# Kernel tuning notes

Hardware: AMD Instinct MI355X
Metric: run time of the kernel (lower is better)

The kernel has to match this reference:

```python
import jax, jax.numpy as jnp
import numpy as np
import math

DIM = 4096
N_HEADS = 32
N_KV_HEADS = 8
HEAD_DIM = DIM // N_HEADS          # 128
N_REP = N_HEADS // N_KV_HEADS      # 4
BATCH = 2
SEQ = 2048
ROPE_THETA = 10000.0


def rope_cos_sin(seq_len, head_dim, theta=ROPE_THETA):
    # matches precompute_freqs_cis: freqs over even indices, outer with positions
    inv_freq = 1.0 / (theta ** (jnp.arange(0, head_dim, 2, dtype=jnp.float32) / head_dim))
    t = jnp.arange(seq_len, dtype=jnp.float32)
    ang = jnp.outer(t, inv_freq)          # [S, head_dim//2]
    return jnp.cos(ang), jnp.sin(ang)


def apply_rope(x, cos, sin):
    # x: [B, S, H, D]; consecutive pairs (x0, x1) form complex numbers (view_as_complex)
    x0 = x[..., 0::2]
    x1 = x[..., 1::2]
    c = cos[None, :, None, :]
    s = sin[None, :, None, :]
    r0 = x0 * c - x1 * s
    r1 = x0 * s + x1 * c
    return jnp.stack([r0, r1], axis=-1).reshape(x.shape)


def setup_inputs() -> dict:
    key = jax.random.key(0)
    ks = jax.random.split(key, 5)
    scale = 1.0 / math.sqrt(DIM)
    return {
        "x": jax.random.normal(ks[0], (BATCH, SEQ, DIM), dtype=jnp.float32),
        "wq": jax.random.normal(ks[1], (DIM, N_HEADS * HEAD_DIM), dtype=jnp.float32) * scale,
        "wk": jax.random.normal(ks[2], (DIM, N_KV_HEADS * HEAD_DIM), dtype=jnp.float32) * scale,
        "wv": jax.random.normal(ks[3], (DIM, N_KV_HEADS * HEAD_DIM), dtype=jnp.float32) * scale,
        "wo": jax.random.normal(ks[4], (N_HEADS * HEAD_DIM, DIM), dtype=jnp.float32) * scale,
        "start_pos": 0,
    }


def reference(x, wq, wk, wv, wo, start_pos):
    B, S, _ = x.shape
    # projections
    q = (x @ wq).reshape(B, S, N_HEADS, HEAD_DIM)
    k = (x @ wk).reshape(B, S, N_KV_HEADS, HEAD_DIM)
    v = (x @ wv).reshape(B, S, N_KV_HEADS, HEAD_DIM)
    # RoPE on q, k (training path: full-sequence freqs)
    cos, sin = rope_cos_sin(S, HEAD_DIM)
    q = apply_rope(q, cos, sin)
    k = apply_rope(k, cos, sin)
    # GQA: repeat_kv expands kv heads by n_rep
    k = jnp.repeat(k, N_REP, axis=2)  # [B, S, H, D]
    v = jnp.repeat(v, N_REP, axis=2)
    # [B, H, S, D]
    q = q.transpose(0, 2, 1, 3)
    k = k.transpose(0, 2, 1, 3)
    v = v.transpose(0, 2, 1, 3)
    scores = jnp.einsum("bhqd,bhkd->bhqk", q, k) / math.sqrt(HEAD_DIM)
    # causal mask: -inf above diagonal
    mask = jnp.triu(jnp.full((S, S), float("-inf"), dtype=scores.dtype), k=1)
    scores = scores + mask[None, None]
    attn = jax.nn.softmax(scores.astype(jnp.float32), axis=-1).astype(q.dtype)
    out = jnp.einsum("bhqk,bhkd->bhqd", attn, v)
    out = out.transpose(0, 2, 1, 3).reshape(B, S, N_HEADS * HEAD_DIM)
    return out @ wo
```

## Files before the change

### kernel.cpp

```cpp
#include <hip/hip_runtime.h>

#define DIM 4096
#define HD 128
#define NH 32
#define NKV 8
#define SEQ 2048
#define BATCH 2
#define MTOT (BATCH*SEQ)
#define GK DIM

typedef __bf16 bf16;
typedef __bf16 bf16x4 __attribute__((ext_vector_type(4)));
typedef __bf16 bf16x8 __attribute__((ext_vector_type(8)));
typedef float f32x4 __attribute__((ext_vector_type(4)));

#define NL2T (-13.287712379549449f / 64.f)

__device__ __forceinline__ void gload_lds16(const void* g, void* l) {
    __builtin_amdgcn_global_load_lds(
        (const __attribute__((address_space(1))) void*)g,
        (__attribute__((address_space(3))) void*)l, 16, 0, 0);
}

__device__ __forceinline__ void tconv64_tile(const float* __restrict__ in,
                                             bf16* __restrict__ out,
                                             int N, int K, int bx, int by,
                                             float t[64][65], int tid) {
    int rr = tid >> 4;
    int cc = (tid & 15) * 4;
    const float* ip = in + ((size_t)(by * 64 + rr)) * N + bx * 64 + cc;
#pragma unroll
    for (int p = 0; p < 4; ++p) {
        float4 v = *(const float4*)(ip + (size_t)p * 16 * N);
        t[rr + p * 16][cc + 0] = v.x;
        t[rr + p * 16][cc + 1] = v.y;
        t[rr + p * 16][cc + 2] = v.z;
        t[rr + p * 16][cc + 3] = v.w;
    }
    __syncthreads();
#pragma unroll
    for (int p = 0; p < 4; ++p) {
        int n = rr + p * 16;
        bf16x4 o;
#pragma unroll
        for (int j = 0; j < 4; ++j) o[j] = (bf16)t[cc + j][n];
        *(bf16x4*)(out + (size_t)(bx * 64 + n) * K + by * 64 + cc) = o;
    }
}

__global__ __launch_bounds__(256) void prep(const float* __restrict__ x,
                                            const float* __restrict__ wq,
                                            const float* __restrict__ wk,
                                            const float* __restrict__ wv,
                                            bf16* __restrict__ xb,
                                            bf16* __restrict__ wqt,
                                            bf16* __restrict__ wkt,
                                            bf16* __restrict__ wvt) {
    __shared__ float t[64][65];
    const int bid = blockIdx.x, tid = threadIdx.x;
    if (bid < 8192) {
        int i = bid * 256 + tid;
        const float4* p = (const float4*)(x + (size_t)i * 8);
        float4 a = p[0], b = p[1];
        bf16x8 v;
        v[0]=(bf16)a.x; v[1]=(bf16)a.y; v[2]=(bf16)a.z; v[3]=(bf16)a.w;
        v[4]=(bf16)b.x; v[5]=(bf16)b.y; v[6]=(bf16)b.z; v[7]=(bf16)b.w;
        *(bf16x8*)(xb + (size_t)i * 8) = v;
    } else if (bid < 8192 + 4096) {
        int b2 = bid - 8192;
        tconv64_tile(wq, wqt, DIM, DIM, b2 & 63, b2 >> 6, t, tid);
    } else if (bid < 8192 + 4096 + 1024) {
        int b2 = bid - (8192 + 4096);
        tconv64_tile(wk, wkt, 1024, DIM, b2 & 15, b2 >> 4, t, tid);
    } else {
        int b2 = bid - (8192 + 4096 + 1024);
        tconv64_tile(wv, wvt, 1024, DIM, b2 & 15, b2 >> 4, t, tid);
    }
}

__global__ __launch_bounds__(256) void tconv64(const float* __restrict__ in,
                                               bf16* __restrict__ out, int N, int K) {
    __shared__ float t[64][65];
    tconv64_tile(in, out, N, K, blockIdx.x, blockIdx.y, t, threadIdx.x);
}

__global__ __launch_bounds__(256, 2) void gemm_kv(const bf16* __restrict__ xb,
                                                  const bf16* __restrict__ wkt,
                                                  const bf16* __restrict__ wvt,
                                                  bf16* __restrict__ kb,
                                                  bf16* __restrict__ vtb) {
    __shared__ alignas(16) bf16 sA[2][128 * 32];
    __shared__ alignas(16) bf16 sB[2][128 * 32];
    const int tid = threadIdx.x;
    const int lane = tid & 63, wid = tid >> 6;
    const int wm = wid >> 1, wn = wid & 1;

    const bf16 *A, *Bt;
    bf16* out0;
    int N, m0, n0;
    const int bid = blockIdx.x;
    const bool isK = (bid < 256);
    if (isK) {
        A = xb; Bt = wkt; out0 = kb; N = 1024;
        m0 = (bid >> 3) * 128; n0 = (bid & 7) * 128;
    } else {
        int b2 = bid - 256;
        A = wvt; Bt = xb; out0 = vtb; N = MTOT;
        m0 = (b2 >> 5) * 128; n0 = (b2 & 31) * 128;
    }

    auto stage = [&](int buf, int kt) {
#pragma unroll
        for (int it = 0; it < 2; ++it) {
            int slot = it * 256 + tid;
            int row = slot >> 2, s = slot & 3;
            gload_lds16(A + (size_t)(m0 + row) * GK + kt * 32 + s * 8, &sA[buf][slot * 8]);
            gload_lds16(Bt + (size_t)(n0 + row) * GK + kt * 32 + s * 8, &sB[buf][slot * 8]);
        }
    };

    f32x4 acc[4][4] = {};
    stage(0, 0);
    __syncthreads();
    int cur = 0;
    for (int kt = 0; kt < GK / 32; ++kt) {
        if (kt + 1 < GK / 32) stage(cur ^ 1, kt + 1);
        bf16x8 bF[4], aF[4];
#pragma unroll
        for (int i = 0; i < 4; ++i)
            bF[i] = *(const bf16x8*)&sB[cur][(wn * 64 + i * 16 + (lane & 15)) * 32 + (lane >> 4) * 8];
#pragma unroll
        for (int i = 0; i < 4; ++i)
            aF[i] = *(const bf16x8*)&sA[cur][(wm * 64 + i * 16 + (lane & 15)) * 32 + (lane >> 4) * 8];
#pragma unroll
        for (int mi = 0; mi < 4; ++mi)
#pragma unroll
            for (int ni = 0; ni < 4; ++ni)
                acc[mi][ni] = __builtin_amdgcn_mfma_f32_16x16x32_bf16(aF[mi], bF[ni], acc[mi][ni], 0, 0, 0);
        __syncthreads();
        cur ^= 1;
    }

    const int lrow = lane & 15;
    if (isK) {
        float inv4[4];
#pragma unroll
        for (int ni = 0; ni < 4; ++ni) {
            int d = (wn * 64 + ni * 16 + lrow) & 127;
            inv4[ni] = exp2f(NL2T * (float)(d >> 1));
        }
        const bool ev = (lrow & 1) == 0;
#pragma unroll
        for (int mi = 0; mi < 4; ++mi)
#pragma unroll
            for (int ni = 0; ni < 4; ++ni)
#pragma unroll
                for (int r = 0; r < 4; ++r) {
                    int row = m0 + wm * 64 + mi * 16 + (lane >> 4) * 4 + r;
                    int col = n0 + wn * 64 + ni * 16 + lrow;
                    float v = acc[mi][ni][r];
                    float p = __shfl_xor(v, 1, 64);
                    float ang = (float)(row & (SEQ - 1)) * inv4[ni];
                    float sn = __sinf(ang), cs = __cosf(ang);
                    float o = v * cs + (ev ? -p * sn : p * sn);
                    out0[(size_t)row * N + col] = (bf16)o;
                }
    } else {
#pragma unroll
        for (int mi = 0; mi < 4; ++mi)
#pragma unroll
            for (int ni = 0; ni < 4; ++ni)
#pragma unroll
                for (int r = 0; r < 4; ++r) {
                    int row = m0 + wm * 64 + mi * 16 + (lane >> 4) * 4 + r;
                    int col = n0 + wn * 64 + ni * 16 + lrow;
                    out0[(size_t)row * N + col] = (bf16)acc[mi][ni][r];
                }
    }
}

template <int MODE>
__global__ __launch_bounds__(512, 2) void gemm8(const bf16* __restrict__ A,
                                                const bf16* __restrict__ Bt,
                                                void* __restrict__ outp, int N,
                                                float oscale) {
    __shared__ alignas(16) char sA[2][2][16384];
    __shared__ alignas(16) char sB[2][2][16384];
    const int tid = threadIdx.x, lane = tid & 63;
    const int wid = tid >> 6;
    const int wm = wid >> 2, wn = wid & 3;
    const int m0 = blockIdx.y * 256, n0 = blockIdx.x * 256;
    const int lrow = lane & 15, hc = lane >> 4;
    const int rowbase = ((lrow >> 1) * 128) +
                        (((((lrow & 1) << 2) | hc) ^ (lrow >> 1)) << 4);
    const int NT = GK / 64;

    auto stageR = [&](int t, int kh) {
#pragma unroll
        for (int it = 0; it < 2; ++it) {
            int sl = it * 512 + tid;
            int PRr = sl >> 3, ps = sl & 7;
            int lsl = ps ^ (PRr & 7);
            int r = PRr * 2 + (lsl >> 2);
            int cc = lsl & 3;
            size_t koff = (size_t)t * 64 + kh * 32 + cc * 8;
            gload_lds16(A + (size_t)(m0 + r) * GK + koff, &sA[t & 1][kh][sl * 16]);
            gload_lds16(Bt + (size_t)(n0 + r) * GK + koff, &sB[t & 1][kh][sl * 16]);
        }
    };

    f32x4 acc[8][4] = {};
    bf16x8 af[8], bfr[4];

    auto phread = [&](int t, int kh) {
        const char* Ab = &sA[t & 1][kh][0];
        const char* Bb = &sB[t & 1][kh][0];
#pragma unroll
        for (int ni = 0; ni < 4; ++ni)
            bfr[ni] = *(const bf16x8*)(Bb + wn * 4096 + ni * 1024 + rowbase);
#pragma unroll
        for (int mi = 0; mi < 8; ++mi)
            af[mi] = *(const bf16x8*)(Ab + wm * 8192 + mi * 1024 + rowbase);
    };
    auto phmfma = [&]() {
        __builtin_amdgcn_s_barrier();
        asm volatile("s_waitcnt lgkmcnt(0)" ::: "memory");
        __builtin_amdgcn_sched_barrier(0);
        __builtin_amdgcn_s_setprio(1);
#pragma unroll
        for (int mi = 0; mi < 8; ++mi)
#pragma unroll
            for (int ni = 0; ni < 4; ++ni)
                acc[mi][ni] = __builtin_amdgcn_mfma_f32_16x16x32_bf16(af[mi], bfr[ni], acc[mi][ni], 0, 0, 0);
        __builtin_amdgcn_s_setprio(0);
    };

    stageR(0, 0); stageR(0, 1);
    asm volatile("s_waitcnt vmcnt(4)" ::: "memory");
    __builtin_amdgcn_s_barrier();

    for (int t = 0; t < NT; ++t) {
#pragma unroll
        for (int kh = 0; kh < 2; ++kh) {
            phread(t, kh);
            if (t + 1 < NT) {
                stageR(t + 1, kh);
                asm volatile("s_waitcnt vmcnt(4)" ::: "memory");
            } else {
                asm volatile("s_waitcnt vmcnt(0)" ::: "memory");
            }
            phmfma();
        }
    }

    if constexpr (MODE == 1) {
        float inv4[4];
#pragma unroll
        for (int ni = 0; ni < 4; ++ni) {
            int d = ((wn & 1) * 64 + ni * 16 + lrow) & 127;
            inv4[ni] = exp2f(NL2T * (float)(d >> 1));
        }
        const bool ev = (lrow & 1) == 0;
#pragma unroll
        for (int mi = 0; mi < 8; ++mi)
#pragma unroll
            for (int ni = 0; ni < 4; ++ni)
#pragma unroll
                for (int r = 0; r < 4; ++r) {
                    int row = m0 + wm * 128 + mi * 16 + hc * 4 + r;
                    int col = n0 + wn * 64 + ni * 16 + lrow;
                    float v = acc[mi][ni][r];
                    float p = __shfl_xor(v, 1, 64);
                    float ang = (float)(row & (SEQ - 1)) * inv4[ni];
                    float sn = __sinf(ang), cs = __cosf(ang);
                    float o = v * cs + (ev ? -p * sn : p * sn);
                    ((bf16*)outp)[(size_t)row * N + col] = (bf16)(o * oscale);
                }
    } else {
#pragma unroll
        for (int mi = 0; mi < 8; ++mi)
#pragma unroll
            for (int ni = 0; ni < 4; ++ni)
#pragma unroll
                for (int r = 0; r < 4; ++r) {
                    int row = m0 + wm * 128 + mi * 16 + hc * 4 + r;
                    int col = n0 + wn * 64 + ni * 16 + lrow;
                    if constexpr (MODE == 2)
                        ((float*)outp)[(size_t)row * N + col] = acc[mi][ni][r];
                    else
                        ((bf16*)outp)[(size_t)row * N + col] = (bf16)acc[mi][ni][r];
                }
    }
}

__global__ __launch_bounds__(512, 4) void attn_fwd(const bf16* __restrict__ q,
                                                   const bf16* __restrict__ k,
                                                   const bf16* __restrict__ vt,
                                                   bf16* __restrict__ o) {
    __shared__ alignas(16) bf16 sK[2][64 * 128];
    __shared__ alignas(16) bf16 sV[2][128 * 64];
    __shared__ alignas(16) bf16 sP[8][16 * 64];
    const int tid = threadIdx.x, lane = tid & 63, wid = tid >> 6;
    const int bi = blockIdx.x;
    const int pr = bi & 7;
    const int h = (bi >> 3) & 31;
    const int b = bi >> 8;
    const int kvh = h >> 2;

    const bf16* kb0 = k + (size_t)b * SEQ * (NKV * HD) + kvh * HD;
    const bf16* vb0 = vt + (size_t)(kvh * HD) * MTOT + (size_t)b * SEQ;

    auto stage = [&](int bf, int tt) {
#pragma unroll
        for (int it = 0; it < 2; ++it) {
            int slot = it * 512 + tid;
            int row = slot >> 4, s = slot & 15;
            gload_lds16(kb0 + (size_t)(tt * 64 + row) * (NKV * HD) + ((s ^ (row & 7)) * 8),
                        &sK[bf][slot * 8]);
        }
#pragma unroll
        for (int it = 0; it < 2; ++it) {
            int slot = it * 512 + tid;
            int row = slot >> 3, s = slot & 7;
            gload_lds16(vb0 + (size_t)row * MTOT + tt * 64 + ((s ^ (row & 7)) * 8),
                        &sV[bf][slot * 8]);
        }
    };

    auto pass = [&](int qt) {
        const int qb0 = qt * 128;
        const int nt = 2 * qt + 2;
        const int qw = qb0 + wid * 16;
        const bf16* qp = q + ((size_t)(b * SEQ + qw + (lane & 15))) * DIM
                           + h * HD + (lane >> 4) * 8;
        bf16x8 aQ[4];
#pragma unroll
        for (int ks = 0; ks < 4; ++ks) aQ[ks] = *(const bf16x8*)(qp + ks * 32);

        f32x4 accO[8] = {};
        float m_r = -1e30f, l_r = 0.f;
        const int qglob = qw + (lane & 15);
        char* pb = (char*)&sP[wid][0];
        const int q7s = (lane & 7) << 4;
        const int hi = lane >> 4;

        stage(0, 0);
        __syncthreads();
        int cur = 0;
        for (int tt = 0; tt < nt; ++tt) {
            if (tt + 1 < nt) stage(cur ^ 1, tt + 1);
            if (tt * 64 <= qw) {
                f32x4 accS[4] = {};
#pragma unroll
                for (int nt2 = 0; nt2 < 4; ++nt2) {
                    int kr = nt2 * 16 + (lane & 15);
#pragma unroll
                    for (int ks = 0; ks < 4; ++ks) {
                        int slog = ks * 4 + hi;
                        bf16x8 bK = *(const bf16x8*)&sK[cur][kr * 128 + ((slog ^ (kr & 7)) * 8)];
                        accS[nt2] = __builtin_amdgcn_mfma_f32_16x16x32_bf16(bK, aQ[ks], accS[nt2], 0, 0, 0);
                    }
                }

                const bool diag = (tt * 64 + 63 > qw);
                float mx = -1e30f;
                if (diag) {
                    const int kvb = tt * 64 + hi * 4;
#pragma unroll
                    for (int nt2 = 0; nt2 < 4; ++nt2)
#pragma unroll
                        for (int r = 0; r < 4; ++r) {
                            float v = accS[nt2][r];
                            if (kvb + nt2 * 16 + r > qglob) v = -1e30f;
                            accS[nt2][r] = v;
                            mx = fmaxf(mx, v);
                        }
                } else {
#pragma unroll
                    for (int nt2 = 0; nt2 < 4; ++nt2)
#pragma unroll
                        for (int r = 0; r < 4; ++r) mx = fmaxf(mx, accS[nt2][r]);
                }
                mx = fmaxf(mx, __shfl_xor(mx, 16, 64));
                mx = fmaxf(mx, __shfl_xor(mx, 32, 64));

                if (!__all(mx <= m_r + 8.f)) {
                    float mn = fmaxf(m_r, mx);
                    float al = __builtin_amdgcn_exp2f(m_r - mn);
                    m_r = mn;
                    l_r *= al;
                    float al4[4];
#pragma unroll
                    for (int r = 0; r < 4; ++r) al4[r] = __shfl(al, hi * 4 + r, 64);
#pragma unroll
                    for (int d2 = 0; d2 < 8; ++d2)
#pragma unroll
                        for (int r = 0; r < 4; ++r) accO[d2][r] *= al4[r];
                }

                float rs = 0.f;
#pragma unroll
                for (int nt2 = 0; nt2 < 4; ++nt2)
#pragma unroll
                    for (int r = 0; r < 4; ++r) {
                        float p = __builtin_amdgcn_exp2f(accS[nt2][r] - m_r);
                        accS[nt2][r] = p;
                        rs += p;
                    }
                l_r += rs;

#pragma unroll
                for (int nt2 = 0; nt2 < 4; ++nt2) {
                    bf16x4 pv;
                    pv[0] = (bf16)accS[nt2][0]; pv[1] = (bf16)accS[nt2][1];
                    pv[2] = (bf16)accS[nt2][2]; pv[3] = (bf16)accS[nt2][3];
                    *(bf16x4*)(pb + (lane & 15) * 128 + ((nt2 * 32 + hi * 8) ^ q7s)) = pv;
                }

                bf16x8 aP[2];
#pragma unroll
                for (int kk = 0; kk < 2; ++kk)
                    aP[kk] = *(const bf16x8*)(pb + (lane & 15) * 128 + ((kk * 64 + hi * 16) ^ q7s));
#pragma unroll
                for (int d2 = 0; d2 < 8; ++d2) {
#pragma unroll
                    for (int kk = 0; kk < 2; ++kk) {
                        int dv = d2 * 16 + (lane & 15);
                        int phys = (kk * 4 + hi) ^ (dv & 7);
                        bf16x8 bV = *(const bf16x8*)&sV[cur][dv * 64 + phys * 8];
                        accO[d2] = __builtin_amdgcn_mfma_f32_16x16x32_bf16(aP[kk], bV, accO[d2], 0, 0, 0);
                    }
                }
            }
            __syncthreads();
            cur ^= 1;
        }

        l_r += __shfl_xor(l_r, 16, 64);
        l_r += __shfl_xor(l_r, 32, 64);
        float linv[4];
#pragma unroll
        for (int r = 0; r < 4; ++r) linv[r] = 1.f / __shfl(l_r, hi * 4 + r, 64);
        size_t orow = (size_t)(b * SEQ + qb0 + wid * 16 + hi * 4) * DIM
                    + h * HD + (lane & 15);
#pragma unroll
        for (int d2 = 0; d2 < 8; ++d2)
#pragma unroll
            for (int r = 0; r < 4; ++r)
                o[orow + (size_t)r * DIM + d2 * 16] = (bf16)(accO[d2][r] * linv[r]);
    };

    pass(pr);
    pass(15 - pr);
}

extern "C" void kernel_launch(void* const* d_in, const int* in_sizes, int n_in,
                              void* d_out, int out_size, void* d_ws, size_t ws_size,
                              hipStream_t stream) {
    const float* x  = (const float*)d_in[0];
    const float* wq = (const float*)d_in[1];
    const float* wk = (const float*)d_in[2];
    const float* wv = (const float*)d_in[3];
    const float* wo = (const float*)d_in[4];
    float* out = (float*)d_out;

    char* ws = (char*)d_ws;
    size_t off = 0;
    bf16* xb  = (bf16*)(ws + off); off += (size_t)MTOT * DIM * 2;
    bf16* wqt = (bf16*)(ws + off); off += (size_t)DIM * DIM * 2;
    bf16* wkt = (bf16*)(ws + off); off += (size_t)1024 * DIM * 2;
    bf16* wvt = (bf16*)(ws + off); off += (size_t)1024 * DIM * 2;
    bf16* qb  = (bf16*)(ws + off); off += (size_t)MTOT * DIM * 2;
    bf16* kb  = (bf16*)(ws + off); off += (size_t)MTOT * 1024 * 2;
    bf16* vtb = (bf16*)(ws + off); off += (size_t)MTOT * 1024 * 2;
    bf16* ao = xb;

    const float SCALE2 = 0.08838834764831845f * 1.44269504088896340f;

    prep<<<8192 + 4096 + 1024 + 1024, 256, 0, stream>>>(x, wq, wk, wv, xb, wqt, wkt, wvt);

    gemm8<1><<<dim3(DIM / 256, MTOT / 256), 512, 0, stream>>>(xb, wqt, qb, DIM, SCALE2);

    gemm_kv<<<512, 256, 0, stream>>>(xb, wkt, wvt, kb, vtb);

    tconv64<<<dim3(DIM / 64, DIM / 64), 256, 0, stream>>>(wo, wqt, DIM, DIM);

    attn_fwd<<<BATCH * NH * 8, 512, 0, stream>>>(qb, kb, vtb, ao);

    gemm8<2><<<dim3(DIM / 256, MTOT / 256), 512, 0, stream>>>(ao, wqt, out, DIM, 1.0f);
}
```

Before: 508.0 us.

## Give each attention wave two 16-row query tiles to reuse K/V fragments

The attention kernel moves from 8 waves per block with 16 query rows each to 4 waves per block with 32 query rows each, split into two 16-row sub-tiles. Each K or V fragment read from shared memory now feeds two MFMAs, halving shared-memory read traffic per unit of matrix work. Softmax state, masking, the P buffer and the output write are duplicated per sub-tile, and the staging loop now uses 256 threads. The cost is more registers per wave and half as many waves per block, which lowers occupancy and latency hiding; causal skipping also now works at 32-row granularity.

```diff
diff --git a/kernel.cpp b/kernel.cpp
--- a/kernel.cpp
+++ b/kernel.cpp
@@ -293,13 +293,13 @@
     }
 }
 
-__global__ __launch_bounds__(512, 4) void attn_fwd(const bf16* __restrict__ q,
+__global__ __launch_bounds__(256, 2) void attn_fwd(const bf16* __restrict__ q,
                                                    const bf16* __restrict__ k,
                                                    const bf16* __restrict__ vt,
                                                    bf16* __restrict__ o) {
     __shared__ alignas(16) bf16 sK[2][64 * 128];
     __shared__ alignas(16) bf16 sV[2][128 * 64];
-    __shared__ alignas(16) bf16 sP[8][16 * 64];
+    __shared__ alignas(16) bf16 sP[4][32 * 64];
     const int tid = threadIdx.x, lane = tid & 63, wid = tid >> 6;
     const int bi = blockIdx.x;
     const int pr = bi & 7;
@@ -312,15 +312,15 @@
 
     auto stage = [&](int bf, int tt) {
 #pragma unroll
-        for (int it = 0; it < 2; ++it) {
-            int slot = it * 512 + tid;
+        for (int it = 0; it < 4; ++it) {
+            int slot = it * 256 + tid;
             int row = slot >> 4, s = slot & 15;
             gload_lds16(kb0 + (size_t)(tt * 64 + row) * (NKV * HD) + ((s ^ (row & 7)) * 8),
                         &sK[bf][slot * 8]);
         }
 #pragma unroll
-        for (int it = 0; it < 2; ++it) {
-            int slot = it * 512 + tid;
+        for (int it = 0; it < 4; ++it) {
+            int slot = it * 256 + tid;
             int row = slot >> 3, s = slot & 7;
             gload_lds16(vb0 + (size_t)row * MTOT + tt * 64 + ((s ^ (row & 7)) * 8),
                         &sV[bf][slot * 8]);
@@ -330,19 +330,21 @@
     auto pass = [&](int qt) {
         const int qb0 = qt * 128;
         const int nt = 2 * qt + 2;
-        const int qw = qb0 + wid * 16;
-        const bf16* qp = q + ((size_t)(b * SEQ + qw + (lane & 15))) * DIM
-                           + h * HD + (lane >> 4) * 8;
-        bf16x8 aQ[4];
-#pragma unroll
-        for (int ks = 0; ks < 4; ++ks) aQ[ks] = *(const bf16x8*)(qp + ks * 32);
-
-        f32x4 accO[8] = {};
-        float m_r = -1e30f, l_r = 0.f;
-        const int qglob = qw + (lane & 15);
+        const int qw = qb0 + wid * 32;
+        const int qg = lane & 15, hi = lane >> 4;
+        const bf16* qp = q + ((size_t)(b * SEQ + qw + qg)) * DIM + h * HD + hi * 8;
+        bf16x8 aQ[2][4];
+#pragma unroll
+        for (int qh = 0; qh < 2; ++qh)
+#pragma unroll
+            for (int ks = 0; ks < 4; ++ks)
+                aQ[qh][ks] = *(const bf16x8*)(qp + (size_t)qh * 16 * DIM + ks * 32);
+
+        f32x4 accO[8][2] = {};
+        float m_r[2] = {-1e30f, -1e30f};
+        float l_r[2] = {0.f, 0.f};
         char* pb = (char*)&sP[wid][0];
-        const int q7s = (lane & 7) << 4;
-        const int hi = lane >> 4;
+        const int q7s = (qg & 7) << 4;
 
         stage(0, 0);
         __syncthreads();
@@ -350,85 +352,113 @@
         for (int tt = 0; tt < nt; ++tt) {
             if (tt + 1 < nt) stage(cur ^ 1, tt + 1);
             if (tt * 64 <= qw) {
-                f32x4 accS[4] = {};
+                f32x4 accS[4][2] = {};
 #pragma unroll
                 for (int nt2 = 0; nt2 < 4; ++nt2) {
-                    int kr = nt2 * 16 + (lane & 15);
+                    int kr = nt2 * 16 + qg;
 #pragma unroll
                     for (int ks = 0; ks < 4; ++ks) {
                         int slog = ks * 4 + hi;
                         bf16x8 bK = *(const bf16x8*)&sK[cur][kr * 128 + ((slog ^ (kr & 7)) * 8)];
-                        accS[nt2] = __builtin_amdgcn_mfma_f32_16x16x32_bf16(bK, aQ[ks], accS[nt2], 0, 0, 0);
+                        accS[nt2][0] = __builtin_amdgcn_mfma_f32_16x16x32_bf16(bK, aQ[0][ks], accS[nt2][0], 0, 0, 0);
+                        accS[nt2][1] = __builtin_amdgcn_mfma_f32_16x16x32_bf16(bK, aQ[1][ks], accS[nt2][1], 0, 0, 0);
                     }
                 }
 
                 const bool diag = (tt * 64 + 63 > qw);
-                float mx = -1e30f;
+                float mx[2] = {-1e30f, -1e30f};
                 if (diag) {
                     const int kvb = tt * 64 + hi * 4;
 #pragma unroll
                     for (int nt2 = 0; nt2 < 4; ++nt2)
 #pragma unroll
                         for (int r = 0; r < 4; ++r) {
-                            float v = accS[nt2][r];
-                            if (kvb + nt2 * 16 + r > qglob) v = -1e30f;
-                            accS[nt2][r] = v;
-                            mx = fmaxf(mx, v);
+                            int kvv = kvb + nt2 * 16 + r;
+#pragma unroll
+                            for (int qh = 0; qh < 2; ++qh) {
+                                float v = accS[nt2][qh][r];
+                                if (kvv > qw + qh * 16 + qg) v = -1e30f;
+                                accS[nt2][qh][r] = v;
+                                mx[qh] = fmaxf(mx[qh], v);
+                            }
                         }
                 } else {
 #pragma unroll
                     for (int nt2 = 0; nt2 < 4; ++nt2)
 #pragma unroll
-                        for (int r = 0; r < 4; ++r) mx = fmaxf(mx, accS[nt2][r]);
-                }
-                mx = fmaxf(mx, __shfl_xor(mx, 16, 64));
-                mx = fmaxf(mx, __shfl_xor(mx, 32, 64));
-
-                if (!__all(mx <= m_r + 8.f)) {
-                    float mn = fmaxf(m_r, mx);
-                    float al = __builtin_amdgcn_exp2f(m_r - mn);
-                    m_r = mn;
-                    l_r *= al;
-                    float al4[4];
-#pragma unroll
-                    for (int r = 0; r < 4; ++r) al4[r] = __shfl(al, hi * 4 + r, 64);
+                        for (int r = 0; r < 4; ++r)
+#pragma unroll
+                            for (int qh = 0; qh < 2; ++qh)
+                                mx[qh] = fmaxf(mx[qh], accS[nt2][qh][r]);
+                }
+#pragma unroll
+                for (int qh = 0; qh < 2; ++qh) {
+                    mx[qh] = fmaxf(mx[qh], __shfl_xor(mx[qh], 16, 64));
+                    mx[qh] = fmaxf(mx[qh], __shfl_xor(mx[qh], 32, 64));
+                }
+
+                if (!__all(mx[0] <= m_r[0] + 8.f && mx[1] <= m_r[1] + 8.f)) {
+                    float al[2], al4[2][4];
+#pragma unroll
+                    for (int qh = 0; qh < 2; ++qh) {
+                        float mn = fmaxf(m_r[qh], mx[qh]);
+                        al[qh] = __builtin_amdgcn_exp2f(m_r[qh] - mn);
+                        m_r[qh] = mn;
+                        l_r[qh] *= al[qh];
+                    }
+#pragma unroll
+                    for (int qh = 0; qh < 2; ++qh)
+#pragma unroll
+                        for (int r = 0; r < 4; ++r)
+                            al4[qh][r] = __shfl(al[qh], hi * 4 + r, 64);
 #pragma unroll
                     for (int d2 = 0; d2 < 8; ++d2)
 #pragma unroll
-                        for (int r = 0; r < 4; ++r) accO[d2][r] *= al4[r];
-                }
-
-                float rs = 0.f;
+                        for (int qh = 0; qh < 2; ++qh)
+#pragma unroll
+                            for (int r = 0; r < 4; ++r)
+                                accO[d2][qh][r] *= al4[qh][r];
+                }
+
+#pragma unroll
+                for (int qh = 0; qh < 2; ++qh) {
+                    float rs = 0.f;
+#pragma unroll
+                    for (int nt2 = 0; nt2 < 4; ++nt2)
+#pragma unroll
+                        for (int r = 0; r < 4; ++r) {
+                            float p = __builtin_amdgcn_exp2f(accS[nt2][qh][r] - m_r[qh]);
+                            accS[nt2][qh][r] = p;
+                            rs += p;
+                        }
+                    l_r[qh] += rs;
+                }
+
 #pragma unroll
                 for (int nt2 = 0; nt2 < 4; ++nt2)
 #pragma unroll
-                    for (int r = 0; r < 4; ++r) {
-                        float p = __builtin_amdgcn_exp2f(accS[nt2][r] - m_r);
-                        accS[nt2][r] = p;
-                        rs += p;
+                    for (int qh = 0; qh < 2; ++qh) {
+                        bf16x4 pv;
+                        pv[0] = (bf16)accS[nt2][qh][0]; pv[1] = (bf16)accS[nt2][qh][1];
+                        pv[2] = (bf16)accS[nt2][qh][2]; pv[3] = (bf16)accS[nt2][qh][3];
+                        *(bf16x4*)(pb + (qh * 16 + qg) * 128 + ((nt2 * 32 + hi * 8) ^ q7s)) = pv;
                     }
-                l_r += rs;
-
-#pragma unroll
-                for (int nt2 = 0; nt2 < 4; ++nt2) {
-                    bf16x4 pv;
-                    pv[0] = (bf16)accS[nt2][0]; pv[1] = (bf16)accS[nt2][1];
-                    pv[2] = (bf16)accS[nt2][2]; pv[3] = (bf16)accS[nt2][3];
-                    *(bf16x4*)(pb + (lane & 15) * 128 + ((nt2 * 32 + hi * 8) ^ q7s)) = pv;
-                }
-
-                bf16x8 aP[2];
+
+                bf16x8 aP[2][2];
 #pragma unroll
                 for (int kk = 0; kk < 2; ++kk)
-                    aP[kk] = *(const bf16x8*)(pb + (lane & 15) * 128 + ((kk * 64 + hi * 16) ^ q7s));
+#pragma unroll
+                    for (int qh = 0; qh < 2; ++qh)
+                        aP[kk][qh] = *(const bf16x8*)(pb + (qh * 16 + qg) * 128 + ((kk * 64 + hi * 16) ^ q7s));
 #pragma unroll
                 for (int d2 = 0; d2 < 8; ++d2) {
 #pragma unroll
                     for (int kk = 0; kk < 2; ++kk) {
-                        int dv = d2 * 16 + (lane & 15);
+                        int dv = d2 * 16 + qg;
                         int phys = (kk * 4 + hi) ^ (dv & 7);
                         bf16x8 bV = *(const bf16x8*)&sV[cur][dv * 64 + phys * 8];
-                        accO[d2] = __builtin_amdgcn_mfma_f32_16x16x32_bf16(aP[kk], bV, accO[d2], 0, 0, 0);
+                        accO[d2][0] = __builtin_amdgcn_mfma_f32_16x16x32_bf16(aP[kk][0], bV, accO[d2][0], 0, 0, 0);
+                        accO[d2][1] = __builtin_amdgcn_mfma_f32_16x16x32_bf16(aP[kk][1], bV, accO[d2][1], 0, 0, 0);
                     }
                 }
             }
@@ -436,18 +466,25 @@
             cur ^= 1;
         }
 
-        l_r += __shfl_xor(l_r, 16, 64);
-        l_r += __shfl_xor(l_r, 32, 64);
-        float linv[4];
-#pragma unroll
-        for (int r = 0; r < 4; ++r) linv[r] = 1.f / __shfl(l_r, hi * 4 + r, 64);
-        size_t orow = (size_t)(b * SEQ + qb0 + wid * 16 + hi * 4) * DIM
-                    + h * HD + (lane & 15);
-#pragma unroll
-        for (int d2 = 0; d2 < 8; ++d2)
+        float linv[2][4];
+#pragma unroll
+        for (int qh = 0; qh < 2; ++qh) {
+            l_r[qh] += __shfl_xor(l_r[qh], 16, 64);
+            l_r[qh] += __shfl_xor(l_r[qh], 32, 64);
 #pragma unroll
             for (int r = 0; r < 4; ++r)
-                o[orow + (size_t)r * DIM + d2 * 16] = (bf16)(accO[d2][r] * linv[r]);
+                linv[qh][r] = 1.f / __shfl(l_r[qh], hi * 4 + r, 64);
+        }
+#pragma unroll
+        for (int qh = 0; qh < 2; ++qh) {
+            size_t orow = (size_t)(b * SEQ + qw + qh * 16 + hi * 4) * DIM
+                        + h * HD + qg;
+#pragma unroll
+            for (int d2 = 0; d2 < 8; ++d2)
+#pragma unroll
+                for (int r = 0; r < 4; ++r)
+                    o[orow + (size_t)r * DIM + d2 * 16] = (bf16)(accO[d2][qh][r] * linv[qh][r]);
+        }
     };
 
     pass(pr);
@@ -485,7 +522,7 @@
 
     tconv64<<<dim3(DIM / 64, DIM / 64), 256, 0, stream>>>(wo, wqt, DIM, DIM);
 
-    attn_fwd<<<BATCH * NH * 8, 512, 0, stream>>>(qb, kb, vtb, ao);
+    attn_fwd<<<BATCH * NH * 8, 256, 0, stream>>>(qb, kb, vtb, ao);
 
     gemm8<2><<<dim3(DIM / 256, MTOT / 256), 512, 0, stream>>>(ao, wqt, out, DIM, 1.0f);
 }
```

Measured after the change: 502.7 us. About the same (-1.1%).
